# Optimization experiments

Hardware: AMD Instinct MI355X
Metric: run time of the kernel (lower is better)

## Reference

```python
import jax, jax.numpy as jnp
import numpy as np

FRAME_LEN = 1024  # matches init_kwargs


def setup_inputs() -> dict:
    key = jax.random.key(0)
    audio = jax.random.normal(key, (16, 512000), dtype=jnp.float32)
    return {"audio": audio}


def reference(audio):
    frame_len = FRAME_LEN
    hop = frame_len // 2
    N = hop
    n0 = (N + 1) / 2.0
    pad = frame_len // 4  # 'same' padding

    # scipy.signal.cosine window: sin(pi*(n+0.5)/M)
    window = jnp.asarray(
        np.sin(np.pi * (np.arange(frame_len) + 0.5) / frame_len), dtype=jnp.float32
    )
    pre_twiddle = jnp.exp(
        -1j * jnp.pi * jnp.arange(frame_len) / frame_len
    ).astype(jnp.complex64)
    post_twiddle = jnp.exp(
        -1j * jnp.pi * n0 * (jnp.arange(N) + 0.5) / N
    ).astype(jnp.complex64)

    a = jnp.pad(audio, ((0, 0), (pad, pad)))
    T = a.shape[-1]
    L = (T - frame_len) // hop + 1
    # overlapping frames via gather: [L, frame_len] index grid
    idx = jnp.arange(L)[:, None] * hop + jnp.arange(frame_len)[None, :]
    x = a[:, idx] * window  # [B, L, frame_len]

    X = jnp.fft.fft(x.astype(jnp.complex64) * pre_twiddle, axis=-1)[..., :N]
    res = X * post_twiddle * np.sqrt(1.0 / N)
    return jnp.real(res) * np.sqrt(2.0)  # [B, L, N]
```

## Files before the change

### kernel.cpp

```cpp
#include <hip/hip_runtime.h>
#include <stdint.h>

typedef unsigned short u16;
typedef short bf16x8 __attribute__((ext_vector_type(8)));
typedef float f32x4 __attribute__((ext_vector_type(4)));

#define PI_F 3.14159265358979323846f
#define NSAMP 512000
#define MROWS 16000
#define K2 512
#define NKOUT 512
#define BK 64
#define NBLK 500

__device__ __forceinline__ u16 f2bf(float f) {
  uint32_t x = __float_as_uint(f);
  return (u16)((x + 0x7fffu + ((x >> 16) & 1u)) >> 16);
}
__device__ __forceinline__ float bf2f(u16 u) {
  return __uint_as_float(((uint32_t)u) << 16);
}

__global__ void build_basis(u16* __restrict__ bt_hi, u16* __restrict__ bt_lo) {
  int idx = blockIdx.x * 256 + threadIdx.x;
  int k = idx >> 9, m = idx & 511;
  int n = m & 255;
  int P = ((2 * n + 513) * (2 * k + 1)) & 4095;
  float ang = PI_F * (float)P / 2048.0f;
  float v = (m < 256) ? cosf(ang) : ((k & 1) ? sinf(ang) : -sinf(ang));
  v *= 0.0625f;
  u16 hi = f2bf(v);
  bt_hi[idx] = hi;
  bt_lo[idx] = f2bf(v - bf2f(hi));
}

__global__ void build_window(float* __restrict__ wsin, float* __restrict__ wcos) {
  int n = threadIdx.x;
  float ph = PI_F * (float)(2 * n + 1) / 2048.0f;
  wsin[n] = sinf(ph);
  wcos[n] = cosf(ph);
}

__device__ __forceinline__ void gl_lds16(const u16* g, u16* l) {
  __builtin_amdgcn_global_load_lds(
      (const __attribute__((address_space(1))) uint32_t*)g,
      (__attribute__((address_space(3))) uint32_t*)l, 16, 0, 0);
}

__global__ __launch_bounds__(256, 2) void mdct_mfma(
    const float* __restrict__ audio,
    const u16* __restrict__ bt_hi, const u16* __restrict__ bt_lo,
    const float* __restrict__ wsin_g, const float* __restrict__ wcos_g,
    float* __restrict__ out) {
  __shared__ u16 Ahi[8192], Alo[8192], Bhi[8192], Blo[8192];
  __shared__ float Wsin[256], Wcos[256];

  const int tid = threadIdx.x;
  const int lane = tid & 63;
  const int wid = tid >> 6;
  const int wr = wid >> 1, wcol = wid & 1;

  int orig = (int)blockIdx.x;
  int xcd = orig & 7, bidx = orig >> 3;
  int wgid = (xcd < 4 ? xcd * 63 : 252 + (xcd - 4) * 62) + bidx;
  const int m0 = (wgid >> 2) * 128;
  const int n0 = (wgid & 3) * 128;

  if (tid < 64)
    ((float4*)Wsin)[tid] = ((const float4*)wsin_g)[tid];
  else if (tid < 128)
    ((float4*)Wcos)[tid - 64] = ((const float4*)wcos_g)[tid - 64];

  const float* aptr[4];
  int base_[4], sl8_[4], awoff_[4], beoff_[4], bdst_[4];
#pragma unroll
  for (int s = 0; s < 4; ++s) {
    int c = tid + 256 * s;
    int row = c >> 3, slot = c & 7;
    int m = m0 + row;
    int b = m / 1000, l = m - b * 1000;
    aptr[s] = audio + (size_t)b * NSAMP;
    base_[s] = l * 512 - 256;
    sl8_[s] = slot * 8;
    int sw = slot ^ (row & 7);
    awoff_[s] = row * 128 + sw * 16;
    beoff_[s] = (n0 + row) * K2 + sw * 8;
    bdst_[s] = c * 8;
  }

  f32x4 acc[4][4];
#pragma unroll
  for (int mi = 0; mi < 4; ++mi)
#pragma unroll
    for (int ni = 0; ni < 4; ++ni)
      acc[mi][ni] = (f32x4){0.f, 0.f, 0.f, 0.f};

  for (int kk = 0; kk < K2; kk += BK) {
    __syncthreads();

#pragma unroll
    for (int s = 0; s < 4; ++s) {
      gl_lds16(bt_hi + beoff_[s] + kk, Bhi + bdst_[s]);
      gl_lds16(bt_lo + beoff_[s] + kk, Blo + bdst_[s]);
    }

    const bool isU = (kk < 256);
#pragma unroll
    for (int s = 0; s < 4; ++s) {
      int n0c = kk + sl8_[s] - (isU ? 0 : 256);
      int tf = base_[s] + (isU ? n0c : 512 + n0c);
      int tr = base_[s] + (isU ? 504 - n0c : 1016 - n0c);
      float4 f0 = make_float4(0.f, 0.f, 0.f, 0.f), f1 = f0, r0 = f0, r1 = f0;
      if ((unsigned)tf < (unsigned)NSAMP) {
        f0 = *(const float4*)(aptr[s] + tf);
        f1 = *(const float4*)(aptr[s] + tf + 4);
      }
      if ((unsigned)tr < (unsigned)NSAMP) {
        r0 = *(const float4*)(aptr[s] + tr);
        r1 = *(const float4*)(aptr[s] + tr + 4);
      }
      float4 s0 = *(const float4*)&Wsin[n0c], s1 = *(const float4*)&Wsin[n0c + 4];
      float4 c0 = *(const float4*)&Wcos[n0c], c1 = *(const float4*)&Wcos[n0c + 4];
      float xf[8] = {f0.x, f0.y, f0.z, f0.w, f1.x, f1.y, f1.z, f1.w};
      float xr[8] = {r0.x, r0.y, r0.z, r0.w, r1.x, r1.y, r1.z, r1.w};
      float sw_[8] = {s0.x, s0.y, s0.z, s0.w, s1.x, s1.y, s1.z, s1.w};
      float cw_[8] = {c0.x, c0.y, c0.z, c0.w, c1.x, c1.y, c1.z, c1.w};
      bf16x8 vh, vl;
#pragma unroll
      for (int j = 0; j < 8; ++j) {
        float uv = isU ? (xf[j] * sw_[j] - xr[7 - j] * cw_[j])
                       : (xf[j] * cw_[j] + xr[7 - j] * sw_[j]);
        u16 h = f2bf(uv);
        vh[j] = (short)h;
        vl[j] = (short)f2bf(uv - bf2f(h));
      }
      *(bf16x8*)((char*)Ahi + awoff_[s]) = vh;
      *(bf16x8*)((char*)Alo + awoff_[s]) = vl;
    }

    __syncthreads();

#pragma unroll
    for (int kb = 0; kb < 2; ++kb) {
      bf16x8 ah[4], al[4], bh[4], bl[4];
#pragma unroll
      for (int mi = 0; mi < 4; ++mi) {
        int row = wr * 64 + mi * 16 + (lane & 15);
        int off = row * 128 + ((((kb << 2) | (lane >> 4)) ^ (row & 7)) << 4);
        ah[mi] = *(const bf16x8*)((const char*)Ahi + off);
        al[mi] = *(const bf16x8*)((const char*)Alo + off);
      }
#pragma unroll
      for (int ni = 0; ni < 4; ++ni) {
        int col = wcol * 64 + ni * 16 + (lane & 15);
        int off = col * 128 + ((((kb << 2) | (lane >> 4)) ^ (col & 7)) << 4);
        bh[ni] = *(const bf16x8*)((const char*)Bhi + off);
        bl[ni] = *(const bf16x8*)((const char*)Blo + off);
      }
#pragma unroll
      for (int mi = 0; mi < 4; ++mi)
#pragma unroll
        for (int ni = 0; ni < 4; ++ni) {
          acc[mi][ni] = __builtin_amdgcn_mfma_f32_16x16x32_bf16(ah[mi], bh[ni], acc[mi][ni], 0, 0, 0);
          acc[mi][ni] = __builtin_amdgcn_mfma_f32_16x16x32_bf16(ah[mi], bl[ni], acc[mi][ni], 0, 0, 0);
          acc[mi][ni] = __builtin_amdgcn_mfma_f32_16x16x32_bf16(al[mi], bh[ni], acc[mi][ni], 0, 0, 0);
        }
    }
  }

#pragma unroll
  for (int mi = 0; mi < 4; ++mi) {
    int row0 = m0 + wr * 64 + mi * 16 + ((lane >> 4) << 2);
#pragma unroll
    for (int ni = 0; ni < 4; ++ni) {
      int col = n0 + wcol * 64 + ni * 16 + (lane & 15);
      float* p = out + (size_t)row0 * NKOUT + col;
      f32x4 v = acc[mi][ni];
      p[0] = v[0];
      p[NKOUT] = v[1];
      p[2 * NKOUT] = v[2];
      p[3 * NKOUT] = v[3];
    }
  }
}

__global__ void mdct_naive(const float* __restrict__ audio, float* __restrict__ out) {
  int idx = blockIdx.x * 256 + threadIdx.x;
  if (idx >= MROWS * NKOUT) return;
  int k = idx & (NKOUT - 1);
  int m = idx >> 9;
  int b = m / 1000, l = m - b * 1000;
  const float* a = audio + (size_t)b * NSAMP;
  float s = 0.f;
  for (int n = 0; n < 1024; ++n) {
    int t = l * 512 + n - 256;
    float x = ((unsigned)t < (unsigned)NSAMP) ? a[t] : 0.f;
    float w = sinf(PI_F * (float)(2 * n + 1) / 2048.0f);
    int P = ((2 * n + 513) * (2 * k + 1)) & 4095;
    s += x * w * cosf(PI_F * (float)P / 2048.0f);
  }
  out[idx] = 0.0625f * s;
}

extern "C" void kernel_launch(void* const* d_in, const int* in_sizes, int n_in,
                              void* d_out, int out_size, void* d_ws, size_t ws_size,
                              hipStream_t stream) {
  const float* audio = (const float*)d_in[0];
  float* out = (float*)d_out;
  size_t tbl = (size_t)NKOUT * K2;
  size_t need = tbl * 2 * sizeof(u16) + 512 * sizeof(float);
  if (d_ws != nullptr && ws_size >= need) {
    u16* bt_hi = (u16*)d_ws;
    u16* bt_lo = bt_hi + tbl;
    float* wsin = (float*)(bt_lo + tbl);
    float* wcos = wsin + 256;
    build_basis<<<(NKOUT * K2) / 256, 256, 0, stream>>>(bt_hi, bt_lo);
    build_window<<<1, 256, 0, stream>>>(wsin, wcos);
    mdct_mfma<<<NBLK, 256, 0, stream>>>(audio, bt_hi, bt_lo, wsin, wcos, out);
  } else {
    mdct_naive<<<(MROWS * NKOUT + 255) / 256, 256, 0, stream>>>(audio, out);
  }
}
```

Measured before the change: 116.3 us.

## Load MFMA operands directly into registers, dropping LDS staging and barriers

```diff
diff --git a/kernel.cpp b/kernel.cpp
--- a/kernel.cpp
+++ b/kernel.cpp
@@ -2,6 +2,7 @@
 #include <stdint.h>
 
 typedef unsigned short u16;
+typedef uint32_t u32;
 typedef short bf16x8 __attribute__((ext_vector_type(8)));
 typedef float f32x4 __attribute__((ext_vector_type(4)));
 
@@ -10,7 +11,6 @@
 #define MROWS 16000
 #define K2 512
 #define NKOUT 512
-#define BK 64
 #define NBLK 500
 
 __device__ __forceinline__ u16 f2bf(float f) {
@@ -41,10 +41,25 @@
   wcos[n] = cosf(ph);
 }
 
-__device__ __forceinline__ void gl_lds16(const u16* g, u16* l) {
-  __builtin_amdgcn_global_load_lds(
-      (const __attribute__((address_space(1))) uint32_t*)g,
-      (__attribute__((address_space(3))) uint32_t*)l, 16, 0, 0);
+__device__ __forceinline__ void split8(const float* u, bf16x8& vh, bf16x8& vl) {
+  u32 h[8], lo[8];
+#pragma unroll
+  for (int j = 0; j < 8; ++j) {
+    u32 x = __float_as_uint(u[j]);
+    h[j] = x & 0xffff0000u;
+    lo[j] = __float_as_uint(u[j] - __uint_as_float(h[j]));
+  }
+  union {
+    u32 w[4];
+    bf16x8 v;
+  } H, L;
+#pragma unroll
+  for (int j = 0; j < 4; ++j) {
+    H.w[j] = __builtin_amdgcn_perm(h[2 * j + 1], h[2 * j], 0x07060302u);
+    L.w[j] = __builtin_amdgcn_perm(lo[2 * j + 1], lo[2 * j], 0x07060302u);
+  }
+  vh = H.v;
+  vl = L.v;
 }
 
 __global__ __launch_bounds__(256, 2) void mdct_mfma(
@@ -52,13 +67,18 @@
     const u16* __restrict__ bt_hi, const u16* __restrict__ bt_lo,
     const float* __restrict__ wsin_g, const float* __restrict__ wcos_g,
     float* __restrict__ out) {
-  __shared__ u16 Ahi[8192], Alo[8192], Bhi[8192], Blo[8192];
   __shared__ float Wsin[256], Wcos[256];
 
   const int tid = threadIdx.x;
   const int lane = tid & 63;
   const int wid = tid >> 6;
   const int wr = wid >> 1, wcol = wid & 1;
+
+  if (tid < 64)
+    ((float4*)Wsin)[tid] = ((const float4*)wsin_g)[tid];
+  else if (tid < 128)
+    ((float4*)Wcos)[tid - 64] = ((const float4*)wcos_g)[tid - 64];
+  __syncthreads();
 
   int orig = (int)blockIdx.x;
   int xcd = orig & 7, bidx = orig >> 3;
@@ -66,26 +86,23 @@
   const int m0 = (wgid >> 2) * 128;
   const int n0 = (wgid & 3) * 128;
 
-  if (tid < 64)
-    ((float4*)Wsin)[tid] = ((const float4*)wsin_g)[tid];
-  else if (tid < 128)
-    ((float4*)Wcos)[tid - 64] = ((const float4*)wcos_g)[tid - 64];
-
-  const float* aptr[4];
-  int base_[4], sl8_[4], awoff_[4], beoff_[4], bdst_[4];
-#pragma unroll
-  for (int s = 0; s < 4; ++s) {
-    int c = tid + 256 * s;
-    int row = c >> 3, slot = c & 7;
-    int m = m0 + row;
+  const float* ap[4];
+  int fb[4];
+#pragma unroll
+  for (int mi = 0; mi < 4; ++mi) {
+    int m = m0 + wr * 64 + mi * 16 + (lane & 15);
     int b = m / 1000, l = m - b * 1000;
-    aptr[s] = audio + (size_t)b * NSAMP;
-    base_[s] = l * 512 - 256;
-    sl8_[s] = slot * 8;
-    int sw = slot ^ (row & 7);
-    awoff_[s] = row * 128 + sw * 16;
-    beoff_[s] = (n0 + row) * K2 + sw * 8;
-    bdst_[s] = c * 8;
+    ap[mi] = audio + (size_t)b * NSAMP;
+    fb[mi] = l * 512 - 256;
+  }
+  const int kc8 = (lane >> 4) * 8;
+
+  const u16 *bhp[4], *blp[4];
+#pragma unroll
+  for (int ni = 0; ni < 4; ++ni) {
+    int col = n0 + wcol * 64 + ni * 16 + (lane & 15);
+    bhp[ni] = bt_hi + (size_t)col * K2 + kc8;
+    blp[ni] = bt_lo + (size_t)col * K2 + kc8;
   }
 
   f32x4 acc[4][4];
@@ -95,76 +112,65 @@
     for (int ni = 0; ni < 4; ++ni)
       acc[mi][ni] = (f32x4){0.f, 0.f, 0.f, 0.f};
 
-  for (int kk = 0; kk < K2; kk += BK) {
-    __syncthreads();
-
-#pragma unroll
-    for (int s = 0; s < 4; ++s) {
-      gl_lds16(bt_hi + beoff_[s] + kk, Bhi + bdst_[s]);
-      gl_lds16(bt_lo + beoff_[s] + kk, Blo + bdst_[s]);
-    }
-
-    const bool isU = (kk < 256);
-#pragma unroll
-    for (int s = 0; s < 4; ++s) {
-      int n0c = kk + sl8_[s] - (isU ? 0 : 256);
-      int tf = base_[s] + (isU ? n0c : 512 + n0c);
-      int tr = base_[s] + (isU ? 504 - n0c : 1016 - n0c);
-      float4 f0 = make_float4(0.f, 0.f, 0.f, 0.f), f1 = f0, r0 = f0, r1 = f0;
+  for (int t = 0; t < 16; ++t) {
+    const bool isU = (t < 8);
+    const int nc = (t & 7) * 32 + kc8;
+
+    bf16x8 bh[4], bl[4];
+#pragma unroll
+    for (int ni = 0; ni < 4; ++ni) {
+      bh[ni] = *(const bf16x8*)(bhp[ni] + t * 32);
+      bl[ni] = *(const bf16x8*)(blp[ni] + t * 32);
+    }
+
+    float4 f0[4], f1[4], r0[4], r1[4];
+#pragma unroll
+    for (int mi = 0; mi < 4; ++mi) {
+      int tf = fb[mi] + (isU ? nc : 512 + nc);
+      int tr = fb[mi] + (isU ? 504 - nc : 1016 - nc);
+      float4 z = make_float4(0.f, 0.f, 0.f, 0.f);
+      f0[mi] = z; f1[mi] = z; r0[mi] = z; r1[mi] = z;
       if ((unsigned)tf < (unsigned)NSAMP) {
-        f0 = *(const float4*)(aptr[s] + tf);
-        f1 = *(const float4*)(aptr[s] + tf + 4);
+        f0[mi] = *(const float4*)(ap[mi] + tf);
+        f1[mi] = *(const float4*)(ap[mi] + tf + 4);
       }
       if ((unsigned)tr < (unsigned)NSAMP) {
-        r0 = *(const float4*)(aptr[s] + tr);
-        r1 = *(const float4*)(aptr[s] + tr + 4);
-      }
-      float4 s0 = *(const float4*)&Wsin[n0c], s1 = *(const float4*)&Wsin[n0c + 4];
-      float4 c0 = *(const float4*)&Wcos[n0c], c1 = *(const float4*)&Wcos[n0c + 4];
-      float xf[8] = {f0.x, f0.y, f0.z, f0.w, f1.x, f1.y, f1.z, f1.w};
-      float xr[8] = {r0.x, r0.y, r0.z, r0.w, r1.x, r1.y, r1.z, r1.w};
-      float sw_[8] = {s0.x, s0.y, s0.z, s0.w, s1.x, s1.y, s1.z, s1.w};
-      float cw_[8] = {c0.x, c0.y, c0.z, c0.w, c1.x, c1.y, c1.z, c1.w};
-      bf16x8 vh, vl;
+        r0[mi] = *(const float4*)(ap[mi] + tr);
+        r1[mi] = *(const float4*)(ap[mi] + tr + 4);
+      }
+    }
+
+    float wA[8], wB[8];
+    {
+      float4 s0 = *(const float4*)&Wsin[nc], s1 = *(const float4*)&Wsin[nc + 4];
+      float4 c0 = *(const float4*)&Wcos[nc], c1 = *(const float4*)&Wcos[nc + 4];
+      float ss[8] = {s0.x, s0.y, s0.z, s0.w, s1.x, s1.y, s1.z, s1.w};
+      float cc[8] = {c0.x, c0.y, c0.z, c0.w, c1.x, c1.y, c1.z, c1.w};
 #pragma unroll
       for (int j = 0; j < 8; ++j) {
-        float uv = isU ? (xf[j] * sw_[j] - xr[7 - j] * cw_[j])
-                       : (xf[j] * cw_[j] + xr[7 - j] * sw_[j]);
-        u16 h = f2bf(uv);
-        vh[j] = (short)h;
-        vl[j] = (short)f2bf(uv - bf2f(h));
-      }
-      *(bf16x8*)((char*)Ahi + awoff_[s]) = vh;
-      *(bf16x8*)((char*)Alo + awoff_[s]) = vl;
-    }
-
-    __syncthreads();
-
-#pragma unroll
-    for (int kb = 0; kb < 2; ++kb) {
-      bf16x8 ah[4], al[4], bh[4], bl[4];
-#pragma unroll
-      for (int mi = 0; mi < 4; ++mi) {
-        int row = wr * 64 + mi * 16 + (lane & 15);
-        int off = row * 128 + ((((kb << 2) | (lane >> 4)) ^ (row & 7)) << 4);
-        ah[mi] = *(const bf16x8*)((const char*)Ahi + off);
-        al[mi] = *(const bf16x8*)((const char*)Alo + off);
-      }
+        wA[j] = isU ? ss[j] : cc[j];
+        wB[j] = isU ? -cc[j] : ss[j];
+      }
+    }
+
+#pragma unroll
+    for (int mi = 0; mi < 4; ++mi) {
+      float xf[8] = {f0[mi].x, f0[mi].y, f0[mi].z, f0[mi].w,
+                     f1[mi].x, f1[mi].y, f1[mi].z, f1[mi].w};
+      float xr[8] = {r0[mi].x, r0[mi].y, r0[mi].z, r0[mi].w,
+                     r1[mi].x, r1[mi].y, r1[mi].z, r1[mi].w};
+      float u[8];
+#pragma unroll
+      for (int j = 0; j < 8; ++j)
+        u[j] = fmaf(xf[j], wA[j], xr[7 - j] * wB[j]);
+      bf16x8 ah, al;
+      split8(u, ah, al);
 #pragma unroll
       for (int ni = 0; ni < 4; ++ni) {
-        int col = wcol * 64 + ni * 16 + (lane & 15);
-        int off = col * 128 + ((((kb << 2) | (lane >> 4)) ^ (col & 7)) << 4);
-        bh[ni] = *(const bf16x8*)((const char*)Bhi + off);
-        bl[ni] = *(const bf16x8*)((const char*)Blo + off);
-      }
-#pragma unroll
-      for (int mi = 0; mi < 4; ++mi)
-#pragma unroll
-        for (int ni = 0; ni < 4; ++ni) {
-          acc[mi][ni] = __builtin_amdgcn_mfma_f32_16x16x32_bf16(ah[mi], bh[ni], acc[mi][ni], 0, 0, 0);
-          acc[mi][ni] = __builtin_amdgcn_mfma_f32_16x16x32_bf16(ah[mi], bl[ni], acc[mi][ni], 0, 0, 0);
-          acc[mi][ni] = __builtin_amdgcn_mfma_f32_16x16x32_bf16(al[mi], bh[ni], acc[mi][ni], 0, 0, 0);
-        }
+        acc[mi][ni] = __builtin_amdgcn_mfma_f32_16x16x32_bf16(ah, bh[ni], acc[mi][ni], 0, 0, 0);
+        acc[mi][ni] = __builtin_amdgcn_mfma_f32_16x16x32_bf16(ah, bl[ni], acc[mi][ni], 0, 0, 0);
+        acc[mi][ni] = __builtin_amdgcn_mfma_f32_16x16x32_bf16(al, bh[ni], acc[mi][ni], 0, 0, 0);
+      }
     }
   }
 
```

After: 164.4 us. +41.3%, slower.

## Split MDCT into fold/split prepass and double-buffered bf16x3 GEMM

Applied to the files above, without the earlier changes.

```diff
diff --git a/kernel.cpp b/kernel.cpp
--- a/kernel.cpp
+++ b/kernel.cpp
@@ -2,6 +2,7 @@
 #include <stdint.h>
 
 typedef unsigned short u16;
+typedef uint32_t u32;
 typedef short bf16x8 __attribute__((ext_vector_type(8)));
 typedef float f32x4 __attribute__((ext_vector_type(4)));
 
@@ -10,7 +11,6 @@
 #define MROWS 16000
 #define K2 512
 #define NKOUT 512
-#define BK 64
 #define NBLK 500
 
 __device__ __forceinline__ u16 f2bf(float f) {
@@ -41,36 +41,197 @@
   wcos[n] = cosf(ph);
 }
 
+__device__ __forceinline__ void split8(const float* u, bf16x8& vh, bf16x8& vl) {
+  u32 h[8], lo[8];
+#pragma unroll
+  for (int j = 0; j < 8; ++j) {
+    u32 x = __float_as_uint(u[j]);
+    h[j] = x & 0xffff0000u;
+    lo[j] = __float_as_uint(u[j] - __uint_as_float(h[j]));
+  }
+  union { u32 w[4]; bf16x8 v; } H, L;
+#pragma unroll
+  for (int j = 0; j < 4; ++j) {
+    H.w[j] = __builtin_amdgcn_perm(h[2 * j + 1], h[2 * j], 0x07060302u);
+    L.w[j] = __builtin_amdgcn_perm(lo[2 * j + 1], lo[2 * j], 0x07060302u);
+  }
+  vh = H.v;
+  vl = L.v;
+}
+
+__global__ __launch_bounds__(256) void fold_split(
+    const float* __restrict__ audio,
+    const float* __restrict__ wsin_g, const float* __restrict__ wcos_g,
+    u16* __restrict__ af_hi, u16* __restrict__ af_lo) {
+  int gid = blockIdx.x * 256 + threadIdx.x;
+  int m = gid >> 6;
+  int k0 = (gid & 63) * 8;
+  bool isU = k0 < 256;
+  int nc = k0 & 255;
+  int b = m / 1000, l = m - b * 1000;
+  const float* ap = audio + (size_t)b * NSAMP;
+  int base = l * 512 - 256;
+  int tf = base + (isU ? nc : 512 + nc);
+  int tr = base + (isU ? 504 - nc : 1016 - nc);
+  float4 z = make_float4(0.f, 0.f, 0.f, 0.f);
+  float4 f0 = z, f1 = z, r0 = z, r1 = z;
+  if ((unsigned)tf < (unsigned)NSAMP) {
+    f0 = *(const float4*)(ap + tf);
+    f1 = *(const float4*)(ap + tf + 4);
+  }
+  if ((unsigned)tr < (unsigned)NSAMP) {
+    r0 = *(const float4*)(ap + tr);
+    r1 = *(const float4*)(ap + tr + 4);
+  }
+  float4 s0 = *(const float4*)(wsin_g + nc), s1 = *(const float4*)(wsin_g + nc + 4);
+  float4 c0 = *(const float4*)(wcos_g + nc), c1 = *(const float4*)(wcos_g + nc + 4);
+  float xf[8] = {f0.x, f0.y, f0.z, f0.w, f1.x, f1.y, f1.z, f1.w};
+  float xr[8] = {r0.x, r0.y, r0.z, r0.w, r1.x, r1.y, r1.z, r1.w};
+  float ss[8] = {s0.x, s0.y, s0.z, s0.w, s1.x, s1.y, s1.z, s1.w};
+  float cc[8] = {c0.x, c0.y, c0.z, c0.w, c1.x, c1.y, c1.z, c1.w};
+  float u[8];
+#pragma unroll
+  for (int j = 0; j < 8; ++j) {
+    float wA = isU ? ss[j] : cc[j];
+    float wB = isU ? -cc[j] : ss[j];
+    u[j] = fmaf(xf[j], wA, xr[7 - j] * wB);
+  }
+  bf16x8 vh, vl;
+  split8(u, vh, vl);
+  size_t o = (size_t)m * K2 + k0;
+  *(bf16x8*)(af_hi + o) = vh;
+  *(bf16x8*)(af_lo + o) = vl;
+}
+
 __device__ __forceinline__ void gl_lds16(const u16* g, u16* l) {
   __builtin_amdgcn_global_load_lds(
       (const __attribute__((address_space(1))) uint32_t*)g,
       (__attribute__((address_space(3))) uint32_t*)l, 16, 0, 0);
 }
 
-__global__ __launch_bounds__(256, 2) void mdct_mfma(
+__global__ __launch_bounds__(256, 2) void mdct_gemm(
+    const u16* __restrict__ af_hi, const u16* __restrict__ af_lo,
+    const u16* __restrict__ bt_hi, const u16* __restrict__ bt_lo,
+    float* __restrict__ out) {
+  __shared__ u16 lds[2][4][4096];
+
+  const int tid = threadIdx.x;
+  const int lane = tid & 63;
+  const int wid = tid >> 6;
+  const int wr = wid >> 1, wcol = wid & 1;
+
+  int orig = (int)blockIdx.x;
+  int xcd = orig & 7, bidx = orig >> 3;
+  int wgid = (xcd < 4 ? xcd * 63 : 252 + (xcd - 4) * 62) + bidx;
+  const int m0 = (wgid >> 2) * 128;
+  const int n0 = (wgid & 3) * 128;
+
+  int asrc[2], bsrc[2];
+#pragma unroll
+  for (int s = 0; s < 2; ++s) {
+    int c = tid + (s << 8);
+    int row = c >> 2, slot = c & 3;
+    int sw = slot ^ ((row >> 1) & 3);
+    asrc[s] = (m0 + row) * K2 + sw * 8;
+    bsrc[s] = (n0 + row) * K2 + sw * 8;
+  }
+
+  int aoff[4], boff[4];
+#pragma unroll
+  for (int mi = 0; mi < 4; ++mi) {
+    int row = wr * 64 + mi * 16 + (lane & 15);
+    aoff[mi] = row * 64 + ((((lane >> 4) ^ ((row >> 1) & 3))) << 4);
+  }
+#pragma unroll
+  for (int ni = 0; ni < 4; ++ni) {
+    int col = wcol * 64 + ni * 16 + (lane & 15);
+    boff[ni] = col * 64 + ((((lane >> 4) ^ ((col >> 1) & 3))) << 4);
+  }
+
+  f32x4 acc[4][4];
+#pragma unroll
+  for (int mi = 0; mi < 4; ++mi)
+#pragma unroll
+    for (int ni = 0; ni < 4; ++ni)
+      acc[mi][ni] = (f32x4){0.f, 0.f, 0.f, 0.f};
+
+  auto STAGE = [&](int buf, int kk) {
+#pragma unroll
+    for (int s = 0; s < 2; ++s) {
+      int c = tid + (s << 8);
+      gl_lds16(af_hi + asrc[s] + kk, &lds[buf][0][c * 8]);
+      gl_lds16(af_lo + asrc[s] + kk, &lds[buf][1][c * 8]);
+      gl_lds16(bt_hi + bsrc[s] + kk, &lds[buf][2][c * 8]);
+      gl_lds16(bt_lo + bsrc[s] + kk, &lds[buf][3][c * 8]);
+    }
+  };
+
+  STAGE(0, 0);
+  __syncthreads();
+
+  for (int t = 0; t < 16; ++t) {
+    const int cur = t & 1;
+    if (t < 15) STAGE(cur ^ 1, (t + 1) * 32);
+
+    bf16x8 ah[4], al[4], bh[4], bl[4];
+#pragma unroll
+    for (int mi = 0; mi < 4; ++mi) {
+      ah[mi] = *(const bf16x8*)((const char*)&lds[cur][0][0] + aoff[mi]);
+      al[mi] = *(const bf16x8*)((const char*)&lds[cur][1][0] + aoff[mi]);
+    }
+#pragma unroll
+    for (int ni = 0; ni < 4; ++ni) {
+      bh[ni] = *(const bf16x8*)((const char*)&lds[cur][2][0] + boff[ni]);
+      bl[ni] = *(const bf16x8*)((const char*)&lds[cur][3][0] + boff[ni]);
+    }
+#pragma unroll
+    for (int mi = 0; mi < 4; ++mi)
+#pragma unroll
+      for (int ni = 0; ni < 4; ++ni) {
+        acc[mi][ni] = __builtin_amdgcn_mfma_f32_16x16x32_bf16(ah[mi], bh[ni], acc[mi][ni], 0, 0, 0);
+        acc[mi][ni] = __builtin_amdgcn_mfma_f32_16x16x32_bf16(ah[mi], bl[ni], acc[mi][ni], 0, 0, 0);
+        acc[mi][ni] = __builtin_amdgcn_mfma_f32_16x16x32_bf16(al[mi], bh[ni], acc[mi][ni], 0, 0, 0);
+      }
+
+    __syncthreads();
+  }
+
+#pragma unroll
+  for (int mi = 0; mi < 4; ++mi) {
+    int row0 = m0 + wr * 64 + mi * 16 + ((lane >> 4) << 2);
+#pragma unroll
+    for (int ni = 0; ni < 4; ++ni) {
+      int col = n0 + wcol * 64 + ni * 16 + (lane & 15);
+      float* p = out + (size_t)row0 * NKOUT + col;
+      f32x4 v = acc[mi][ni];
+      p[0] = v[0];
+      p[NKOUT] = v[1];
+      p[2 * NKOUT] = v[2];
+      p[3 * NKOUT] = v[3];
+    }
+  }
+}
+
+__global__ __launch_bounds__(256, 2) void mdct_fused(
     const float* __restrict__ audio,
     const u16* __restrict__ bt_hi, const u16* __restrict__ bt_lo,
     const float* __restrict__ wsin_g, const float* __restrict__ wcos_g,
     float* __restrict__ out) {
   __shared__ u16 Ahi[8192], Alo[8192], Bhi[8192], Blo[8192];
   __shared__ float Wsin[256], Wcos[256];
-
   const int tid = threadIdx.x;
   const int lane = tid & 63;
   const int wid = tid >> 6;
   const int wr = wid >> 1, wcol = wid & 1;
-
   int orig = (int)blockIdx.x;
   int xcd = orig & 7, bidx = orig >> 3;
   int wgid = (xcd < 4 ? xcd * 63 : 252 + (xcd - 4) * 62) + bidx;
   const int m0 = (wgid >> 2) * 128;
   const int n0 = (wgid & 3) * 128;
-
   if (tid < 64)
     ((float4*)Wsin)[tid] = ((const float4*)wsin_g)[tid];
   else if (tid < 128)
     ((float4*)Wcos)[tid - 64] = ((const float4*)wcos_g)[tid - 64];
-
   const float* aptr[4];
   int base_[4], sl8_[4], awoff_[4], beoff_[4], bdst_[4];
 #pragma unroll
@@ -87,30 +248,27 @@
     beoff_[s] = (n0 + row) * K2 + sw * 8;
     bdst_[s] = c * 8;
   }
-
   f32x4 acc[4][4];
 #pragma unroll
   for (int mi = 0; mi < 4; ++mi)
 #pragma unroll
     for (int ni = 0; ni < 4; ++ni)
       acc[mi][ni] = (f32x4){0.f, 0.f, 0.f, 0.f};
-
-  for (int kk = 0; kk < K2; kk += BK) {
+  for (int kk = 0; kk < K2; kk += 64) {
     __syncthreads();
-
 #pragma unroll
     for (int s = 0; s < 4; ++s) {
       gl_lds16(bt_hi + beoff_[s] + kk, Bhi + bdst_[s]);
       gl_lds16(bt_lo + beoff_[s] + kk, Blo + bdst_[s]);
     }
-
     const bool isU = (kk < 256);
 #pragma unroll
     for (int s = 0; s < 4; ++s) {
       int n0c = kk + sl8_[s] - (isU ? 0 : 256);
       int tf = base_[s] + (isU ? n0c : 512 + n0c);
       int tr = base_[s] + (isU ? 504 - n0c : 1016 - n0c);
-      float4 f0 = make_float4(0.f, 0.f, 0.f, 0.f), f1 = f0, r0 = f0, r1 = f0;
+      float4 z = make_float4(0.f, 0.f, 0.f, 0.f);
+      float4 f0 = z, f1 = z, r0 = z, r1 = z;
       if ((unsigned)tf < (unsigned)NSAMP) {
         f0 = *(const float4*)(aptr[s] + tf);
         f1 = *(const float4*)(aptr[s] + tf + 4);
@@ -123,23 +281,21 @@
       float4 c0 = *(const float4*)&Wcos[n0c], c1 = *(const float4*)&Wcos[n0c + 4];
       float xf[8] = {f0.x, f0.y, f0.z, f0.w, f1.x, f1.y, f1.z, f1.w};
       float xr[8] = {r0.x, r0.y, r0.z, r0.w, r1.x, r1.y, r1.z, r1.w};
-      float sw_[8] = {s0.x, s0.y, s0.z, s0.w, s1.x, s1.y, s1.z, s1.w};
-      float cw_[8] = {c0.x, c0.y, c0.z, c0.w, c1.x, c1.y, c1.z, c1.w};
+      float ss[8] = {s0.x, s0.y, s0.z, s0.w, s1.x, s1.y, s1.z, s1.w};
+      float cc[8] = {c0.x, c0.y, c0.z, c0.w, c1.x, c1.y, c1.z, c1.w};
+      float u[8];
+#pragma unroll
+      for (int j = 0; j < 8; ++j) {
+        float wA = isU ? ss[j] : cc[j];
+        float wB = isU ? -cc[j] : ss[j];
+        u[j] = fmaf(xf[j], wA, xr[7 - j] * wB);
+      }
       bf16x8 vh, vl;
-#pragma unroll
-      for (int j = 0; j < 8; ++j) {
-        float uv = isU ? (xf[j] * sw_[j] - xr[7 - j] * cw_[j])
-                       : (xf[j] * cw_[j] + xr[7 - j] * sw_[j]);
-        u16 h = f2bf(uv);
-        vh[j] = (short)h;
-        vl[j] = (short)f2bf(uv - bf2f(h));
-      }
+      split8(u, vh, vl);
       *(bf16x8*)((char*)Ahi + awoff_[s]) = vh;
       *(bf16x8*)((char*)Alo + awoff_[s]) = vl;
     }
-
     __syncthreads();
-
 #pragma unroll
     for (int kb = 0; kb < 2; ++kb) {
       bf16x8 ah[4], al[4], bh[4], bl[4];
@@ -167,7 +323,6 @@
         }
     }
   }
-
 #pragma unroll
   for (int mi = 0; mi < 4; ++mi) {
     int row0 = m0 + wr * 64 + mi * 16 + ((lane >> 4) << 2);
@@ -208,15 +363,28 @@
   const float* audio = (const float*)d_in[0];
   float* out = (float*)d_out;
   size_t tbl = (size_t)NKOUT * K2;
-  size_t need = tbl * 2 * sizeof(u16) + 512 * sizeof(float);
-  if (d_ws != nullptr && ws_size >= need) {
+  size_t need_mid = tbl * 2 * sizeof(u16) + 512 * sizeof(float);
+  size_t af = (size_t)MROWS * K2;
+  size_t need_full = need_mid + af * 2 * sizeof(u16);
+  if (d_ws != nullptr && ws_size >= need_full) {
+    u16* bt_hi = (u16*)d_ws;
+    u16* bt_lo = bt_hi + tbl;
+    float* wsin = (float*)(bt_lo + tbl);
+    float* wcos = wsin + 256;
+    u16* af_hi = (u16*)(wcos + 256);
+    u16* af_lo = af_hi + af;
+    build_basis<<<(NKOUT * K2) / 256, 256, 0, stream>>>(bt_hi, bt_lo);
+    build_window<<<1, 256, 0, stream>>>(wsin, wcos);
+    fold_split<<<(MROWS * 64) / 256, 256, 0, stream>>>(audio, wsin, wcos, af_hi, af_lo);
+    mdct_gemm<<<NBLK, 256, 0, stream>>>(af_hi, af_lo, bt_hi, bt_lo, out);
+  } else if (d_ws != nullptr && ws_size >= need_mid) {
     u16* bt_hi = (u16*)d_ws;
     u16* bt_lo = bt_hi + tbl;
     float* wsin = (float*)(bt_lo + tbl);
     float* wcos = wsin + 256;
     build_basis<<<(NKOUT * K2) / 256, 256, 0, stream>>>(bt_hi, bt_lo);
     build_window<<<1, 256, 0, stream>>>(wsin, wcos);
-    mdct_mfma<<<NBLK, 256, 0, stream>>>(audio, bt_hi, bt_lo, wsin, wcos, out);
+    mdct_fused<<<NBLK, 256, 0, stream>>>(audio, bt_hi, bt_lo, wsin, wcos, out);
   } else {
     mdct_naive<<<(MROWS * NKOUT + 255) / 256, 256, 0, stream>>>(audio, out);
   }
```

After: 110.3 us. -5.2%, faster.
